# Kernel tuning notes

Hardware: AMD Instinct MI355X
Metric: run time of the kernel (lower is better)

Reference implementation:

```python
import jax, jax.numpy as jnp
import numpy as np

B, C, H, W = 8, 512, 64, 64
CQK = C // 8  # query/key channels

def conv1x1(x, w, b):
    # x: [B,Cin,H,W], w: [Cout,Cin], b: [Cout]
    return jnp.einsum('oi,bihw->bohw', w, x) + b[None, :, None, None]

def setup_inputs() -> dict:
    key = jax.random.key(0)
    ks = jax.random.split(key, 8)
    s_in = 1.0 / np.sqrt(C)
    return {
        'x': jax.random.normal(ks[0], (B, C, H, W), dtype=jnp.float32),
        'wq': jax.random.normal(ks[1], (CQK, C), dtype=jnp.float32) * s_in,
        'bq': jax.random.normal(ks[2], (CQK,), dtype=jnp.float32) * 0.01,
        'wk': jax.random.normal(ks[3], (CQK, C), dtype=jnp.float32) * s_in,
        'bk': jax.random.normal(ks[4], (CQK,), dtype=jnp.float32) * 0.01,
        'wv': jax.random.normal(ks[5], (C, C), dtype=jnp.float32) * s_in,
        'bv': jax.random.normal(ks[6], (C,), dtype=jnp.float32) * 0.01,
        'alpha': jax.random.normal(ks[7], (1,), dtype=jnp.float32) * 0.1,
    }

def reference(x, wq, bq, wk, bk, wv, bv, alpha):
    b, c, h, w = x.shape
    n = h * w
    q = conv1x1(x, wq, bq).reshape(b, CQK, n)   # [B,C/8,N]
    k = conv1x1(x, wk, bk).reshape(b, CQK, n)   # [B,C/8,N]
    v = conv1x1(x, wv, bv).reshape(b, c, n)     # [B,C,N]
    att = jnp.einsum('bck,bcs->bks', q, k)       # [B,N,N]
    att = jax.nn.softmax(att, axis=-1)
    out = jnp.einsum('bcs,bks->bck', v, att)     # [B,C,N]
    out = out.reshape(b, c, h, w)
    return alpha[0] * out + x
```

## Files before the change

kernel.cpp:

```cpp
#include <hip/hip_runtime.h>
#include <hip/hip_bf16.h>
#include <stdint.h>

#define NB 8
#define NC 512
#define NN 4096
#define ND 64

typedef __attribute__((ext_vector_type(8))) short short8;
typedef __attribute__((ext_vector_type(4))) float f32x4;

#define LOG2E 1.44269504088896340736f

static __device__ __forceinline__ uint32_t cvt_pk_bf16(float lo, float hi) {
    uint32_t r;
    asm("v_cvt_pk_bf16_f32 %0, %1, %2" : "=v"(r) : "v"(lo), "v"(hi));
    return r;
}

static __device__ __forceinline__ void barrier_lgkm() {
    asm volatile("s_waitcnt lgkmcnt(0)" ::: "memory");
    __builtin_amdgcn_s_barrier();
    __builtin_amdgcn_sched_barrier(0);
}

__global__ __launch_bounds__(256) void wprep(
    const float* __restrict__ wq, const float* __restrict__ wk,
    const float* __restrict__ wv, unsigned short* __restrict__ Wbf)
{
    const int g = blockIdx.x * 256 + threadIdx.x;
    const int o = g >> 6;
    const int c = (g & 63) << 3;
    const float* src; float sc;
    if (o < 64)       { src = wq + (size_t)o*NC;        sc = LOG2E; }
    else if (o < 128) { src = wk + (size_t)(o-64)*NC;   sc = 1.f; }
    else              { src = wv + (size_t)(o-128)*NC;  sc = 1.f; }
    float4 a = *reinterpret_cast<const float4*>(src + c);
    float4 d = *reinterpret_cast<const float4*>(src + c + 4);
    uint4 r;
    r.x = cvt_pk_bf16(a.x*sc, a.y*sc);
    r.y = cvt_pk_bf16(a.z*sc, a.w*sc);
    r.z = cvt_pk_bf16(d.x*sc, d.y*sc);
    r.w = cvt_pk_bf16(d.z*sc, d.w*sc);
    *reinterpret_cast<uint4*>(Wbf + (size_t)o*NC + c) = r;
}

__global__ __launch_bounds__(256, 2) void qkv_proj(
    const float* __restrict__ x,
    const unsigned short* __restrict__ Wbf,
    const float* __restrict__ bq, const float* __restrict__ bk,
    const float* __restrict__ bv,
    unsigned short* __restrict__ QT, unsigned short* __restrict__ KT,
    unsigned char* __restrict__ V)
{
    const int nblk = blockIdx.x;
    const int b    = blockIdx.y;
    const int t = threadIdx.x;
    const int wid = t >> 6;
    const int l = t & 63;
    const int lg = l >> 4, lr = l & 15;
    const int n0 = nblk * 64;
    const float* xb = x + (size_t)b * NC * NN;

    __shared__ unsigned short XT[2][64][72];

    const int o_base = wid * 160;

    f32x4 acc[10][4];
    #pragma unroll
    for (int mt = 0; mt < 10; ++mt) {
        const int ob = o_base + mt*16;
        #pragma unroll
        for (int bb = 0; bb < 4; ++bb) {
            const int o = ob + lg*4 + bb;
            float bias = (ob < 64) ? bq[o]*LOG2E : (ob < 128) ? bk[o-64] : bv[o-128];
            #pragma unroll
            for (int nt = 0; nt < 4; ++nt) acc[mt][nt][bb] = bias;
        }
    }

    const int cq = (t >> 4) << 2;
    const int n4 = (t & 15) << 2;
    float4 xs0, xs1, xs2, xs3;
    auto xload = [&](int ks) {
        const float* xr = xb + (size_t)(ks*64 + cq)*NN + n0 + n4;
        xs0 = *reinterpret_cast<const float4*>(xr);
        xs1 = *reinterpret_cast<const float4*>(xr + NN);
        xs2 = *reinterpret_cast<const float4*>(xr + 2*(size_t)NN);
        xs3 = *reinterpret_cast<const float4*>(xr + 3*(size_t)NN);
    };
    auto xwrite = [&](int buf) {
        uint2 w;
        w.x = cvt_pk_bf16(xs0.x, xs1.x); w.y = cvt_pk_bf16(xs2.x, xs3.x);
        *reinterpret_cast<uint2*>(&XT[buf][n4+0][cq]) = w;
        w.x = cvt_pk_bf16(xs0.y, xs1.y); w.y = cvt_pk_bf16(xs2.y, xs3.y);
        *reinterpret_cast<uint2*>(&XT[buf][n4+1][cq]) = w;
        w.x = cvt_pk_bf16(xs0.z, xs1.z); w.y = cvt_pk_bf16(xs2.z, xs3.z);
        *reinterpret_cast<uint2*>(&XT[buf][n4+2][cq]) = w;
        w.x = cvt_pk_bf16(xs0.w, xs1.w); w.y = cvt_pk_bf16(xs2.w, xs3.w);
        *reinterpret_cast<uint2*>(&XT[buf][n4+3][cq]) = w;
    };

    xload(0);
    xwrite(0);
    __syncthreads();

    for (int ks = 0; ks < 8; ++ks) {
        const int buf = ks & 1;
        const int c0 = ks * 64;
        if (ks < 7) xload(ks + 1);
        #pragma unroll
        for (int k2 = 0; k2 < 2; ++k2) {
            short8 bf[4];
            #pragma unroll
            for (int nt = 0; nt < 4; ++nt)
                bf[nt] = *reinterpret_cast<const short8*>(&XT[buf][nt*16 + lr][k2*32 + lg*8]);
            #pragma unroll
            for (int mt = 0; mt < 10; ++mt) {
                short8 af = *reinterpret_cast<const short8*>(
                    Wbf + (size_t)(o_base + mt*16 + lr)*NC + c0 + k2*32 + lg*8);
                #pragma unroll
                for (int nt = 0; nt < 4; ++nt)
                    acc[mt][nt] = __builtin_amdgcn_mfma_f32_16x16x32_bf16(af, bf[nt], acc[mt][nt], 0, 0, 0);
            }
        }
        if (ks < 7) xwrite(buf ^ 1);
        __syncthreads();
    }

    #pragma unroll
    for (int mt = 0; mt < 10; ++mt) {
        const int ob = o_base + mt*16;
        const int ol = ob + lg*4;
        #pragma unroll
        for (int nt = 0; nt < 4; ++nt) {
            const int n = n0 + nt*16 + lr;
            if (ob < 128) {
                uint2 pk;
                pk.x = cvt_pk_bf16(acc[mt][nt][0], acc[mt][nt][1]);
                pk.y = cvt_pk_bf16(acc[mt][nt][2], acc[mt][nt][3]);
                unsigned short* dst = (ob < 64) ? (QT + ((size_t)b*NN + n)*ND + ol)
                                                : (KT + ((size_t)b*NN + n)*ND + (ol - 64));
                *reinterpret_cast<uint2*>(dst) = pk;
            } else {
                const int c = ol - 128;
                #pragma unroll
                for (int bb = 0; bb < 4; ++bb) {
                    int v8 = __builtin_amdgcn_cvt_pk_fp8_f32(acc[mt][nt][bb], 0.f, 0, false);
                    V[((size_t)b*NC + c + bb)*NN + n] = (unsigned char)(v8 & 0xff);
                }
            }
        }
    }
}

__global__ __launch_bounds__(1024) void stats(
    const unsigned short* __restrict__ QT,
    const unsigned short* __restrict__ KT,
    float* __restrict__ Mh)
{
    const int bi = blockIdx.x;
    const int b    = bi & 7;
    const int nt   = (bi >> 3) & 15;
    const int half = bi >> 7;
    const int n0 = nt * 256;
    const int t = threadIdx.x;
    const int wid = t >> 6;
    const int l = t & 63;
    const int lg = l >> 4, lr = l & 15;

    __shared__ __align__(16) unsigned short Klds[2*64*64];

    const unsigned short* Qb = QT + ((size_t)b*NN + n0)*ND;
    const unsigned short* Kb = KT + (size_t)b*NN*ND + (size_t)half*2048*ND;

    short8 qf0 = *reinterpret_cast<const short8*>(Qb + (size_t)(16*wid + lr)*ND + lg*8);
    short8 qf1 = *reinterpret_cast<const short8*>(Qb + (size_t)(16*wid + lr)*ND + 32 + lg*8);

    const int krow = t >> 3;
    const int kdst = krow*64 + ((8*(t & 7)) ^ (8*(krow & 7)));
    if (t < 512) {
        short8 k0 = *reinterpret_cast<const short8*>(Kb + (size_t)t*8);
        *reinterpret_cast<short8*>(&Klds[kdst]) = k0;
    }

    const int kswz = 8*(lr & 7);
    f32x4 mr = f32x4{-1e30f, -1e30f, -1e30f, -1e30f};

    barrier_lgkm();

    for (int i = 0; i < 32; ++i) {
        short8 kr;
        if (t < 512 && i < 31)
            kr = *reinterpret_cast<const short8*>(Kb + (size_t)(i+1)*4096 + t*8);

        const unsigned short* kbuf = &Klds[(i & 1)*4096];
        #pragma unroll
        for (int j = 0; j < 4; ++j) {
            const unsigned short* kp = kbuf + (16*j + lr)*64;
            short8 a0 = *reinterpret_cast<const short8*>(kp + ((8*lg) ^ kswz));
            short8 a1 = *reinterpret_cast<const short8*>(kp + ((32 + 8*lg) ^ kswz));
            f32x4 acc = __builtin_amdgcn_mfma_f32_16x16x32_bf16(a0, qf0, f32x4{0.f,0.f,0.f,0.f}, 0, 0, 0);
            acc = __builtin_amdgcn_mfma_f32_16x16x32_bf16(a1, qf1, acc, 0, 0, 0);
            mr[0] = fmaxf(mr[0], acc[0]);
            mr[1] = fmaxf(mr[1], acc[1]);
            mr[2] = fmaxf(mr[2], acc[2]);
            mr[3] = fmaxf(mr[3], acc[3]);
        }
        if (t < 512 && i < 31)
            *reinterpret_cast<short8*>(&Klds[((i+1) & 1)*4096 + kdst]) = kr;
        barrier_lgkm();
    }

    float mx = fmaxf(fmaxf(mr[0], mr[1]), fmaxf(mr[2], mr[3]));
    mx = fmaxf(mx, __shfl_xor(mx, 16));
    mx = fmaxf(mx, __shfl_xor(mx, 32));
    if (lg == 0) Mh[(size_t)half*NB*NN + (size_t)b*NN + n0 + 16*wid + lr] = mx;
}

__global__ __launch_bounds__(512, 2) void attn(
    const unsigned short* __restrict__ QT,
    const unsigned short* __restrict__ KT,
    const unsigned char* __restrict__ V,
    const float* __restrict__ Mh,
    const float* __restrict__ x,
    const float* __restrict__ alpha_p,
    float* __restrict__ out)
{
    const int bi = blockIdx.x;
    const int b  = bi & 7;
    const int n0 = (bi >> 3) * 128;
    const int t = threadIdx.x;
    const int wid = t >> 6;
    const int l = t & 63;
    const int lg = l >> 4, lr = l & 15;

    __shared__ __align__(16) unsigned short Klds[4*64*64];
    __shared__ __align__(16) unsigned char  Plds[4*128*128];
    __shared__ float Ll[128];

    const unsigned short* Qb = QT + ((size_t)b*NN + n0)*ND;
    const unsigned short* Kb = KT + (size_t)b*NN*ND;
    const unsigned char*  Vb = V + ((size_t)b*NC + 64*wid)*NN;

    short8 qf0 = *reinterpret_cast<const short8*>(Qb + (size_t)(16*wid + lr)*ND + lg*8);
    short8 qf1 = *reinterpret_cast<const short8*>(Qb + (size_t)(16*wid + lr)*ND + 32 + lg*8);

    const int nrow = n0 + 16*wid + lr;
    const float Mreg = fmaxf(Mh[(size_t)b*NN + nrow], Mh[(size_t)NB*NN + (size_t)b*NN + nrow]);

    const int krow = t >> 3;
    const int kdst = krow*64 + ((8*(t & 7)) ^ (8*(krow & 7)));

    {
        short8 k0 = *reinterpret_cast<const short8*>(Kb + (size_t)t*8);
        short8 k1 = *reinterpret_cast<const short8*>(Kb + 4096 + (size_t)t*8);
        *reinterpret_cast<short8*>(&Klds[kdst]) = k0;
        *reinterpret_cast<short8*>(&Klds[4096 + kdst]) = k1;
    }

    f32x4 oacc[8][4];
    #pragma unroll
    for (int mt = 0; mt < 8; ++mt)
        #pragma unroll
        for (int ct = 0; ct < 4; ++ct)
            oacc[mt][ct] = f32x4{0.f, 0.f, 0.f, 0.f};

    float lrun = 0.f;

    long vf[4];
    #pragma unroll
    for (int ct = 0; ct < 4; ++ct)
        vf[ct] = *reinterpret_cast<const long*>(Vb + (size_t)(ct*16 + lr)*NN + 8*lg);

    barrier_lgkm();

    const int kswz = 8*(lr & 7);
    const int pswz = 8*lr;
    const int prow = (16*wid + lr) * 128;

    auto PVstep = [&](const unsigned char* pbase, int k2, int s_pref) {
        long vfn[4];
        #pragma unroll
        for (int ct = 0; ct < 4; ++ct)
            vfn[ct] = *reinterpret_cast<const long*>(
                Vb + (size_t)(ct*16 + lr)*NN + s_pref + 8*lg);
        long pf[8];
        #pragma unroll
        for (int mt = 0; mt < 8; ++mt)
            pf[mt] = *reinterpret_cast<const long*>(
                pbase + (16*mt + lr)*128 + ((k2*32 + 8*lg) ^ pswz));
        __builtin_amdgcn_s_setprio(1);
        #pragma unroll
        for (int mt = 0; mt < 8; ++mt)
            #pragma unroll
            for (int ct = 0; ct < 4; ++ct)
                oacc[mt][ct] = __builtin_amdgcn_mfma_f32_16x16x32_fp8_fp8(
                    pf[mt], vf[ct], oacc[mt][ct], 0, 0, 0);
        __builtin_amdgcn_s_setprio(0);
        #pragma unroll
        for (int ct = 0; ct < 4; ++ct) vf[ct] = vfn[ct];
    };

    auto QKt = [&](const unsigned short* kbuf, f32x4 (&sn)[4]) {
        #pragma unroll
        for (int st8 = 0; st8 < 4; ++st8) {
            const unsigned short* kp = kbuf + (16*st8 + lr)*64;
            short8 a0 = *reinterpret_cast<const short8*>(kp + ((8*lg) ^ kswz));
            short8 a1 = *reinterpret_cast<const short8*>(kp + ((32 + 8*lg) ^ kswz));
            sn[st8] = __builtin_amdgcn_mfma_f32_16x16x32_bf16(a0, qf0, f32x4{0.f,0.f,0.f,0.f}, 0, 0, 0);
            sn[st8] = __builtin_amdgcn_mfma_f32_16x16x32_bf16(a1, qf1, sn[st8], 0, 0, 0);
        }
    };

    auto EXPK = [&](const f32x4 (&sn)[4], unsigned char* pb) {
        #pragma unroll
        for (int st8 = 0; st8 < 4; ++st8) {
            float p0 = __builtin_amdgcn_exp2f(sn[st8][0] - Mreg);
            float p1 = __builtin_amdgcn_exp2f(sn[st8][1] - Mreg);
            float p2 = __builtin_amdgcn_exp2f(sn[st8][2] - Mreg);
            float p3 = __builtin_amdgcn_exp2f(sn[st8][3] - Mreg);
            lrun += (p0 + p1) + (p2 + p3);
            int d = __builtin_amdgcn_cvt_pk_fp8_f32(p0, p1, 0, false);
            d = __builtin_amdgcn_cvt_pk_fp8_f32(p2, p3, d, true);
            *reinterpret_cast<int*>(&pb[prow + ((16*st8 + 4*lg) ^ pswz)]) = d;
        }
    };

    {
        f32x4 sn[4];
        QKt(&Klds[0], sn);
        short8 k2r = *reinterpret_cast<const short8*>(Kb + 2*(size_t)4096 + t*8);
        EXPK(sn, Plds);
        QKt(&Klds[4096], sn);
        short8 k3r = *reinterpret_cast<const short8*>(Kb + 3*(size_t)4096 + t*8);
        EXPK(sn, Plds + 16384);
        *reinterpret_cast<short8*>(&Klds[2*4096 + kdst]) = k2r;
        *reinterpret_cast<short8*>(&Klds[3*4096 + kdst]) = k3r;
    }
    barrier_lgkm();

    for (int i = 0; i < 62; i += 2) {
        const int s0a = i * 64;
        const int s0b = s0a + 64;
        const int i4 = (i + 4 < 64) ? i + 4 : 63;
        const int i5 = (i + 5 < 64) ? i + 5 : 63;
        const unsigned char* pA = Plds + (size_t)(i & 3)*16384;
        const unsigned char* pB = Plds + (size_t)((i + 1) & 3)*16384;

        short8 kra = *reinterpret_cast<const short8*>(Kb + (size_t)i4*4096 + t*8);
        f32x4 sn[4];
        QKt(&Klds[((i + 2) & 3)*4096], sn);
        PVstep(pA, 0, s0a + 32);
        EXPK(sn, Plds + (size_t)((i + 2) & 3)*16384);
        PVstep(pA, 1, s0a + 64);
        *reinterpret_cast<short8*>(&Klds[(i & 3)*4096 + kdst]) = kra;

        short8 krb = *reinterpret_cast<const short8*>(Kb + (size_t)i5*4096 + t*8);
        QKt(&Klds[((i + 3) & 3)*4096], sn);
        PVstep(pB, 0, s0b + 32);
        EXPK(sn, Plds + (size_t)((i + 3) & 3)*16384);
        PVstep(pB, 1, s0b + 64);
        *reinterpret_cast<short8*>(&Klds[((i + 1) & 3)*4096 + kdst]) = krb;

        barrier_lgkm();
    }

    {
        const unsigned char* pA = Plds + (size_t)(62 & 3)*16384;
        const unsigned char* pB = Plds + (size_t)(63 & 3)*16384;
        const int s0a = 62 * 64;
        PVstep(pA, 0, s0a + 32);
        PVstep(pA, 1, s0a + 64);
        PVstep(pB, 0, s0a + 96);
        PVstep(pB, 1, s0a);
    }

    lrun += __shfl_xor(lrun, 16);
    lrun += __shfl_xor(lrun, 32);
    if (lg == 0) Ll[16*wid + lr] = lrun;
    __syncthreads();

    const float alpha = alpha_p[0];
    #pragma unroll
    for (int mt = 0; mt < 8; ++mt) {
        float4 l4 = *reinterpret_cast<const float4*>(&Ll[16*mt + 4*lg]);
        float ar0 = alpha / l4.x, ar1 = alpha / l4.y, ar2 = alpha / l4.z, ar3 = alpha / l4.w;
        #pragma unroll
        for (int ct = 0; ct < 4; ++ct) {
            const int c = 64*wid + 16*ct + lr;
            const size_t base = ((size_t)b*NC + c)*NN + n0 + 16*mt + 4*lg;
            float4 x4 = *reinterpret_cast<const float4*>(x + base);
            float4 o4;
            o4.x = oacc[mt][ct][0] * ar0 + x4.x;
            o4.y = oacc[mt][ct][1] * ar1 + x4.y;
            o4.z = oacc[mt][ct][2] * ar2 + x4.z;
            o4.w = oacc[mt][ct][3] * ar3 + x4.w;
            *reinterpret_cast<float4*>(out + base) = o4;
        }
    }
}

extern "C" void kernel_launch(void* const* d_in, const int* in_sizes, int n_in,
                              void* d_out, int out_size, void* d_ws, size_t ws_size,
                              hipStream_t stream) {
    const float* x     = (const float*)d_in[0];
    const float* wq    = (const float*)d_in[1];
    const float* bq    = (const float*)d_in[2];
    const float* wk    = (const float*)d_in[3];
    const float* bk    = (const float*)d_in[4];
    const float* wv    = (const float*)d_in[5];
    const float* bv    = (const float*)d_in[6];
    const float* alpha = (const float*)d_in[7];

    unsigned short* QT = (unsigned short*)d_ws;
    unsigned short* KT = QT + (size_t)NB*NN*ND;
    unsigned char*  V  = (unsigned char*)(KT + (size_t)NB*NN*ND);
    unsigned short* Wbf = (unsigned short*)(V + (size_t)NB*NC*NN);
    float* Mh = (float*)(Wbf + (size_t)640*NC);

    wprep<<<160, 256, 0, stream>>>(wq, wk, wv, Wbf);
    dim3 gA(64, 8);
    qkv_proj<<<gA, 256, 0, stream>>>(x, Wbf, bq, bk, bv, QT, KT, V);
    stats<<<256, 1024, 0, stream>>>(QT, KT, Mh);
    attn<<<NB * (NN/128), 512, 0, stream>>>(QT, KT, V, Mh, x, alpha, (float*)d_out);
}
```

Before: 222.5 us.

## Use 16x16x128 scaled FP8 MFMA for PV with 128-key double-buffered tiles

```diff
diff --git a/kernel.cpp b/kernel.cpp
--- a/kernel.cpp
+++ b/kernel.cpp
@@ -9,6 +9,7 @@
 
 typedef __attribute__((ext_vector_type(8))) short short8;
 typedef __attribute__((ext_vector_type(4))) float f32x4;
+typedef __attribute__((ext_vector_type(8))) int i32x8;
 
 #define LOG2E 1.44269504088896340736f
 
@@ -235,8 +236,8 @@
     const int l = t & 63;
     const int lg = l >> 4, lr = l & 15;
 
-    __shared__ __align__(16) unsigned short Klds[4*64*64];
-    __shared__ __align__(16) unsigned char  Plds[4*128*128];
+    __shared__ __align__(16) unsigned short Klds[2*128*64];
+    __shared__ __align__(16) unsigned char  Plds[2*128*128];
     __shared__ float Ll[128];
 
     const unsigned short* Qb = QT + ((size_t)b*NN + n0)*ND;
@@ -249,14 +250,16 @@
     const int nrow = n0 + 16*wid + lr;
     const float Mreg = fmaxf(Mh[(size_t)b*NN + nrow], Mh[(size_t)NB*NN + (size_t)b*NN + nrow]);
 
-    const int krow = t >> 3;
-    const int kdst = krow*64 + ((8*(t & 7)) ^ (8*(krow & 7)));
+    const int kr0_row = t >> 3;
+    const int kr1_row = 64 + (t >> 3);
+    const int kc0 = kr0_row*64 + ((8*(t & 7)) ^ (8*(kr0_row & 7)));
+    const int kc1 = kr1_row*64 + ((8*(t & 7)) ^ (8*(kr1_row & 7)));
 
     {
-        short8 k0 = *reinterpret_cast<const short8*>(Kb + (size_t)t*8);
-        short8 k1 = *reinterpret_cast<const short8*>(Kb + 4096 + (size_t)t*8);
-        *reinterpret_cast<short8*>(&Klds[kdst]) = k0;
-        *reinterpret_cast<short8*>(&Klds[4096 + kdst]) = k1;
+        short8 a = *reinterpret_cast<const short8*>(Kb + (size_t)t*8);
+        short8 c = *reinterpret_cast<const short8*>(Kb + 4096 + (size_t)t*8);
+        *reinterpret_cast<short8*>(&Klds[kc0]) = a;
+        *reinterpret_cast<short8*>(&Klds[kc1]) = c;
     }
 
     f32x4 oacc[8][4];
@@ -268,113 +271,109 @@
 
     float lrun = 0.f;
 
-    long vf[4];
-    #pragma unroll
-    for (int ct = 0; ct < 4; ++ct)
-        vf[ct] = *reinterpret_cast<const long*>(Vb + (size_t)(ct*16 + lr)*NN + 8*lg);
-
     barrier_lgkm();
 
     const int kswz = 8*(lr & 7);
     const int pswz = 8*lr;
     const int prow = (16*wid + lr) * 128;
 
-    auto PVstep = [&](const unsigned char* pbase, int k2, int s_pref) {
-        long vfn[4];
-        #pragma unroll
-        for (int ct = 0; ct < 4; ++ct)
-            vfn[ct] = *reinterpret_cast<const long*>(
-                Vb + (size_t)(ct*16 + lr)*NN + s_pref + 8*lg);
-        long pf[8];
-        #pragma unroll
-        for (int mt = 0; mt < 8; ++mt)
-            pf[mt] = *reinterpret_cast<const long*>(
-                pbase + (16*mt + lr)*128 + ((k2*32 + 8*lg) ^ pswz));
-        __builtin_amdgcn_s_setprio(1);
-        #pragma unroll
-        for (int mt = 0; mt < 8; ++mt)
-            #pragma unroll
-            for (int ct = 0; ct < 4; ++ct)
-                oacc[mt][ct] = __builtin_amdgcn_mfma_f32_16x16x32_fp8_fp8(
-                    pf[mt], vf[ct], oacc[mt][ct], 0, 0, 0);
-        __builtin_amdgcn_s_setprio(0);
-        #pragma unroll
-        for (int ct = 0; ct < 4; ++ct) vf[ct] = vfn[ct];
-    };
-
-    auto QKt = [&](const unsigned short* kbuf, f32x4 (&sn)[4]) {
-        #pragma unroll
-        for (int st8 = 0; st8 < 4; ++st8) {
-            const unsigned short* kp = kbuf + (16*st8 + lr)*64;
+    auto QKt = [&](const unsigned short* kbuf, int h, f32x4 (&sn)[4]) {
+        #pragma unroll
+        for (int j = 0; j < 4; ++j) {
+            const unsigned short* kp = kbuf + (64*h + 16*j + lr)*64;
             short8 a0 = *reinterpret_cast<const short8*>(kp + ((8*lg) ^ kswz));
             short8 a1 = *reinterpret_cast<const short8*>(kp + ((32 + 8*lg) ^ kswz));
-            sn[st8] = __builtin_amdgcn_mfma_f32_16x16x32_bf16(a0, qf0, f32x4{0.f,0.f,0.f,0.f}, 0, 0, 0);
-            sn[st8] = __builtin_amdgcn_mfma_f32_16x16x32_bf16(a1, qf1, sn[st8], 0, 0, 0);
-        }
-    };
-
-    auto EXPK = [&](const f32x4 (&sn)[4], unsigned char* pb) {
-        #pragma unroll
-        for (int st8 = 0; st8 < 4; ++st8) {
-            float p0 = __builtin_amdgcn_exp2f(sn[st8][0] - Mreg);
-            float p1 = __builtin_amdgcn_exp2f(sn[st8][1] - Mreg);
-            float p2 = __builtin_amdgcn_exp2f(sn[st8][2] - Mreg);
-            float p3 = __builtin_amdgcn_exp2f(sn[st8][3] - Mreg);
+            sn[j] = __builtin_amdgcn_mfma_f32_16x16x32_bf16(a0, qf0, f32x4{0.f,0.f,0.f,0.f}, 0, 0, 0);
+            sn[j] = __builtin_amdgcn_mfma_f32_16x16x32_bf16(a1, qf1, sn[j], 0, 0, 0);
+        }
+    };
+
+    auto EXPK = [&](const f32x4 (&sn)[4], int h, unsigned char* pb) {
+        #pragma unroll
+        for (int j = 0; j < 4; ++j) {
+            float p0 = __builtin_amdgcn_exp2f(sn[j][0] - Mreg);
+            float p1 = __builtin_amdgcn_exp2f(sn[j][1] - Mreg);
+            float p2 = __builtin_amdgcn_exp2f(sn[j][2] - Mreg);
+            float p3 = __builtin_amdgcn_exp2f(sn[j][3] - Mreg);
             lrun += (p0 + p1) + (p2 + p3);
             int d = __builtin_amdgcn_cvt_pk_fp8_f32(p0, p1, 0, false);
             d = __builtin_amdgcn_cvt_pk_fp8_f32(p2, p3, d, true);
-            *reinterpret_cast<int*>(&pb[prow + ((16*st8 + 4*lg) ^ pswz)]) = d;
+            *reinterpret_cast<int*>(&pb[prow + ((64*h + 16*j + 4*lg) ^ pswz)]) = d;
+        }
+    };
+
+    auto VLD1 = [&](int ct, int s0) -> i32x8 {
+        const uint4* vp = reinterpret_cast<const uint4*>(
+            Vb + (size_t)(ct*16 + lr)*NN + s0 + 32*lg);
+        uint4 lo = vp[0], hi = vp[1];
+        i32x8 v;
+        v[0] = lo.x; v[1] = lo.y; v[2] = lo.z; v[3] = lo.w;
+        v[4] = hi.x; v[5] = hi.y; v[6] = hi.z; v[7] = hi.w;
+        return v;
+    };
+
+    auto PV = [&](const unsigned char* pcur, int s0) {
+        #pragma unroll
+        for (int h = 0; h < 2; ++h) {
+            i32x8 v0 = VLD1(2*h, s0);
+            i32x8 v1 = VLD1(2*h + 1, s0);
+            __builtin_amdgcn_s_setprio(1);
+            #pragma unroll
+            for (int mt = 0; mt < 8; ++mt) {
+                const unsigned char* pr = pcur + (16*mt + lr)*128;
+                int2 q0 = *reinterpret_cast<const int2*>(pr + ((32*lg +  0) ^ pswz));
+                int2 q1 = *reinterpret_cast<const int2*>(pr + ((32*lg +  8) ^ pswz));
+                int2 q2 = *reinterpret_cast<const int2*>(pr + ((32*lg + 16) ^ pswz));
+                int2 q3 = *reinterpret_cast<const int2*>(pr + ((32*lg + 24) ^ pswz));
+                i32x8 pf;
+                pf[0] = q0.x; pf[1] = q0.y; pf[2] = q1.x; pf[3] = q1.y;
+                pf[4] = q2.x; pf[5] = q2.y; pf[6] = q3.x; pf[7] = q3.y;
+                oacc[mt][2*h] = __builtin_amdgcn_mfma_scale_f32_16x16x128_f8f6f4(
+                    pf, v0, oacc[mt][2*h], 0, 0, 0, 127, 0, 127);
+                oacc[mt][2*h + 1] = __builtin_amdgcn_mfma_scale_f32_16x16x128_f8f6f4(
+                    pf, v1, oacc[mt][2*h + 1], 0, 0, 0, 127, 0, 127);
+            }
+            __builtin_amdgcn_s_setprio(0);
         }
     };
 
     {
+        short8 ka = *reinterpret_cast<const short8*>(Kb + (size_t)8192 + t*8);
+        short8 kb2 = *reinterpret_cast<const short8*>(Kb + (size_t)8192 + 4096 + t*8);
         f32x4 sn[4];
-        QKt(&Klds[0], sn);
-        short8 k2r = *reinterpret_cast<const short8*>(Kb + 2*(size_t)4096 + t*8);
-        EXPK(sn, Plds);
-        QKt(&Klds[4096], sn);
-        short8 k3r = *reinterpret_cast<const short8*>(Kb + 3*(size_t)4096 + t*8);
-        EXPK(sn, Plds + 16384);
-        *reinterpret_cast<short8*>(&Klds[2*4096 + kdst]) = k2r;
-        *reinterpret_cast<short8*>(&Klds[3*4096 + kdst]) = k3r;
+        QKt(&Klds[0], 0, sn);
+        EXPK(sn, 0, Plds);
+        QKt(&Klds[0], 1, sn);
+        EXPK(sn, 1, Plds);
+        *reinterpret_cast<short8*>(&Klds[8192 + kc0]) = ka;
+        *reinterpret_cast<short8*>(&Klds[8192 + kc1]) = kb2;
     }
     barrier_lgkm();
 
-    for (int i = 0; i < 62; i += 2) {
-        const int s0a = i * 64;
-        const int s0b = s0a + 64;
-        const int i4 = (i + 4 < 64) ? i + 4 : 63;
-        const int i5 = (i + 5 < 64) ? i + 5 : 63;
-        const unsigned char* pA = Plds + (size_t)(i & 3)*16384;
-        const unsigned char* pB = Plds + (size_t)((i + 1) & 3)*16384;
-
-        short8 kra = *reinterpret_cast<const short8*>(Kb + (size_t)i4*4096 + t*8);
+    for (int i = 0; i < 31; ++i) {
+        const int cur = i & 1, nxt = cur ^ 1;
+        const unsigned char* pcur = Plds + cur*16384;
+        unsigned char* pnxt = Plds + nxt*16384;
+        const int ipre = (i + 2 < 32) ? (i + 2) : 31;
+
         f32x4 sn[4];
-        QKt(&Klds[((i + 2) & 3)*4096], sn);
-        PVstep(pA, 0, s0a + 32);
-        EXPK(sn, Plds + (size_t)((i + 2) & 3)*16384);
-        PVstep(pA, 1, s0a + 64);
-        *reinterpret_cast<short8*>(&Klds[(i & 3)*4096 + kdst]) = kra;
-
-        short8 krb = *reinterpret_cast<const short8*>(Kb + (size_t)i5*4096 + t*8);
-        QKt(&Klds[((i + 3) & 3)*4096], sn);
-        PVstep(pB, 0, s0b + 32);
-        EXPK(sn, Plds + (size_t)((i + 3) & 3)*16384);
-        PVstep(pB, 1, s0b + 64);
-        *reinterpret_cast<short8*>(&Klds[((i + 1) & 3)*4096 + kdst]) = krb;
+        QKt(&Klds[nxt*8192], 0, sn);
+        EXPK(sn, 0, pnxt);
+        QKt(&Klds[nxt*8192], 1, sn);
+        EXPK(sn, 1, pnxt);
+
+        short8 ka = *reinterpret_cast<const short8*>(Kb + (size_t)ipre*8192 + t*8);
+        short8 kb2 = *reinterpret_cast<const short8*>(Kb + (size_t)ipre*8192 + 4096 + t*8);
+
+        PV(pcur, i * 128);
+
+        *reinterpret_cast<short8*>(&Klds[cur*8192 + kc0]) = ka;
+        *reinterpret_cast<short8*>(&Klds[cur*8192 + kc1]) = kb2;
 
         barrier_lgkm();
     }
 
-    {
-        const unsigned char* pA = Plds + (size_t)(62 & 3)*16384;
-        const unsigned char* pB = Plds + (size_t)(63 & 3)*16384;
-        const int s0a = 62 * 64;
-        PVstep(pA, 0, s0a + 32);
-        PVstep(pA, 1, s0a + 64);
-        PVstep(pB, 0, s0a + 96);
-        PVstep(pB, 1, s0a);
-    }
+    PV(Plds + 16384, 31 * 128);
 
     lrun += __shfl_xor(lrun, 16);
     lrun += __shfl_xor(lrun, 32);
```

New measurement: 210.1 us, median of 2. 5.6% less time.
